# Kernel optimization log

Measured on AMD Instinct MI355X. Metric: run time of the kernel, lower is better.

The kernel has to match this reference:

```python
import jax, jax.numpy as jnp
import numpy as np

EPS = 1e-5

def conv3x3(x, w):
    return jax.lax.conv_general_dilated(x, w, (1, 1), 'SAME', dimension_numbers=('NCHW', 'OIHW', 'NCHW'))

def bn_relu(x, g, b):
    # BatchNorm2d in training mode (batch stats, biased variance), weight=g, bias=b, then ReLU
    m = jnp.mean(x, axis=(0, 2, 3), keepdims=True)
    v = jnp.var(x, axis=(0, 2, 3), keepdims=True)
    return jax.nn.relu((x - m) * jax.lax.rsqrt(v + EPS) * g[None, :, None, None] + b[None, :, None, None])

def conv1x1(x, w, b):
    return jnp.einsum('bchw,oc->bohw', x, w) + b[None, :, None, None]

def cc_core(q, k, v):
    # criss-cross attention core: row (H) + col (W) energies, -inf on H diagonal, joint softmax
    H = q.shape[2]
    eH = jnp.einsum('bchw,bcgw->bhwg', q, k)          # [B,H,W,H]
    eH = jnp.where(jnp.eye(H, dtype=bool)[None, :, None, :], -jnp.inf, eH)
    eW = jnp.einsum('bchw,bchv->bhwv', q, k)          # [B,H,W,W]
    att = jax.nn.softmax(jnp.concatenate([eH, eW], axis=-1), axis=-1)
    aH, aW = att[..., :H], att[..., H:]
    oH = jnp.einsum('bcgw,bhwg->bchw', v, aH)
    oW = jnp.einsum('bchv,bhwv->bchw', v, aW)
    return oH + oW

def cc_attention(x, qw, qb, kw, kb, vw, vb, gamma):
    return gamma * cc_core(conv1x1(x, qw, qb), conv1x1(x, kw, kb), conv1x1(x, vw, vb)) + x

def my_attention(x, qw, qb, kw, kb, vw, vb, gamma):
    # criss-cross attention over the batch rearranged into a (B//4, B//4) grid
    B, C, H, W = x.shape
    g = B // 4  # requires g*g == B (B=16)
    def to_grid(t):
        return t.reshape(B, -1).T.reshape(1, -1, g, g)
    o = cc_core(to_grid(conv1x1(x, qw, qb)), to_grid(conv1x1(x, kw, kb)), to_grid(conv1x1(x, vw, vb)))
    o = o.reshape(-1, B).T.reshape(B, C, H, W)
    return gamma * o + x

RECURRENCE = 2

def setup_inputs() -> dict:
    B, Cin, H, W = 16, 1024, 48, 48
    C = Cin // 4      # 256 (CC_channels == my_channels)
    C8 = C // 8       # 32
    NC, OC = 21, 512
    ks = iter(jax.random.split(jax.random.key(0), 40))
    def rn(shape, s):
        return jax.random.normal(next(ks), shape, jnp.float32) * s
    def attn_params(p):
        return {p + 'q_w': rn((C8, C), 0.06), p + 'q_b': jnp.zeros((C8,)),
                p + 'k_w': rn((C8, C), 0.06), p + 'k_b': jnp.zeros((C8,)),
                p + 'v_w': rn((C, C), 0.06), p + 'v_b': jnp.zeros((C,))}
    inp = {'x': rn((B, Cin, H, W), 1.0),
           'w_a': rn((C, Cin, 3, 3), 0.015), 'g_a': jnp.ones((C,)), 'b_a': jnp.zeros((C,))}
    inp.update(attn_params('cc'))
    inp['cc_gamma'] = jnp.asarray(0.1, jnp.float32)
    inp.update({'w_b': rn((C, C, 3, 3), 0.03), 'g_b': jnp.ones((C,)), 'b_b': jnp.zeros((C,)),
                'w_m1': rn((C, Cin, 3, 3), 0.015), 'g_m1': jnp.ones((C,)), 'b_m1': jnp.zeros((C,))})
    inp.update(attn_params('my'))
    inp['my_gamma'] = jnp.asarray(0.1, jnp.float32)
    inp.update({'w_m2': rn((C, C, 3, 3), 0.03), 'g_m2': jnp.ones((C,)), 'b_m2': jnp.zeros((C,)),
                'w_c': rn((OC, Cin + 2 * C, 3, 3), 0.012), 'g_c': jnp.ones((OC,)), 'b_c': jnp.zeros((OC,)),
                'w_cls': rn((NC, OC), 0.04), 'b_cls': jnp.zeros((NC,))})
    return inp

def reference(x, w_a, g_a, b_a, ccq_w, ccq_b, cck_w, cck_b, ccv_w, ccv_b, cc_gamma,
              w_b, g_b, b_b, w_m1, g_m1, b_m1, myq_w, myq_b, myk_w, myk_b, myv_w, myv_b, my_gamma,
              w_m2, g_m2, b_m2, w_c, g_c, b_c, w_cls, b_cls):
    cc = bn_relu(conv3x3(x, w_a), g_a, b_a)
    my = bn_relu(conv3x3(x, w_m1), g_m1, b_m1)
    for _ in range(RECURRENCE):
        cc = cc_attention(cc, ccq_w, ccq_b, cck_w, cck_b, ccv_w, ccv_b, cc_gamma)
    for _ in range(RECURRENCE):
        my = my_attention(my, myq_w, myq_b, myk_w, myk_b, myv_w, myv_b, my_gamma)
    cc = bn_relu(conv3x3(cc, w_b), g_b, b_b)
    my = bn_relu(conv3x3(my, w_m2), g_m2, b_m2)
    h = bn_relu(conv3x3(jnp.concatenate([x, cc, my], axis=1), w_c), g_c, b_c)
    return conv1x1(h, w_cls, b_cls)
```

## Files before the change

### kernel.cpp

```cpp
#include <hip/hip_runtime.h>
#include <hip/hip_bf16.h>
#include <math.h>

typedef __hip_bfloat16 bf16;
typedef unsigned short ushort;
typedef __attribute__((ext_vector_type(8))) short bh8;
typedef __attribute__((ext_vector_type(4))) float f4;

#define HHW 48
#define PP  2304
#define MM  36864

__device__ __forceinline__ float ldf(const float* p) { return *p; }
__device__ __forceinline__ float ldf(const bf16* p) { return __bfloat162float(*p); }
__device__ __forceinline__ void stf(float* p, float v) { *p = v; }
__device__ __forceinline__ void stf(bf16* p, float v) { *p = __float2bfloat16(v); }
__device__ __forceinline__ float b2f(ushort u) { return __uint_as_float((unsigned)u << 16); }
__device__ __forceinline__ ushort f2bu(float f) { bf16 h = __float2bfloat16(f); return *(ushort*)&h; }

__device__ __forceinline__ int loff(int row, int col8) {
    return row * 32 + (col8 ^ ((((row) >> 1) & 3) << 3));
}

__device__ __forceinline__ void gl_lds(const ushort* g, ushort* l) {
    __builtin_amdgcn_global_load_lds((const __attribute__((address_space(1))) void*)g,
                                     (__attribute__((address_space(3))) void*)l, 16, 0, 0);
}

__global__ void x2b_k(const float* __restrict__ x, bf16* __restrict__ xb) {
    __shared__ float tile[32][33];
    int b  = blockIdx.z;
    int c0 = blockIdx.y * 32;
    int p0 = blockIdx.x * 32;
    int lp = threadIdx.x & 31;
    int cg = threadIdx.x >> 5;
    #pragma unroll
    for (int j = 0; j < 4; ++j) {
        int c = cg * 4 + j;
        tile[c][lp] = x[((size_t)b * 1024 + c0 + c) * PP + p0 + lp];
    }
    __syncthreads();
    #pragma unroll
    for (int j = 0; j < 4; ++j) {
        int rp = cg * 4 + j;
        xb[((size_t)b * PP + p0 + rp) * 1024 + c0 + lp] = __float2bfloat16(tile[lp][rp]);
    }
}

__global__ void w3b_k(const float* __restrict__ w, bf16* __restrict__ wb, int Cout, int Cin) {
    int idx = blockIdx.x * 256 + threadIdx.x;
    int n = Cout * Cin * 9;
    if (idx >= n) return;
    int kk  = idx / (Cout * Cin);
    int rem = idx - kk * Cout * Cin;
    int co  = rem / Cin;
    int ci  = rem - co * Cin;
    wb[idx] = __float2bfloat16(w[((size_t)co * Cin + ci) * 9 + kk]);
}

__global__ void wqkv_k(const float* __restrict__ qw, const float* __restrict__ kw,
                       const float* __restrict__ vw, bf16* __restrict__ dst) {
    int idx = blockIdx.x * 256 + threadIdx.x;
    if (idx >= 320 * 256) return;
    int r = idx >> 8, c = idx & 255;
    float v = (r < 32) ? qw[r * 256 + c] : (r < 64) ? kw[(r - 32) * 256 + c]
                                                    : vw[(size_t)(r - 64) * 256 + c];
    dst[idx] = __float2bfloat16(v);
}

__global__ void cb_k(const float* __restrict__ qb, const float* __restrict__ kb,
                     const float* __restrict__ vb, float* __restrict__ dst) {
    int i = threadIdx.x;
    dst[i] = (i < 32) ? qb[i] : (i < 64) ? kb[i - 32] : vb[i - 64];
}

__global__ void tw1_k(const float* __restrict__ w, float* __restrict__ wt, int O, int Cm) {
    int idx = blockIdx.x * 256 + threadIdx.x;
    int n = O * Cm;
    if (idx >= n) return;
    int o = idx / Cm;
    int c = idx - o * Cm;
    wt[c * O + o] = w[idx];
}

template<typename OutT>
__global__ __launch_bounds__(256, 2)
void mconv3_k(const bf16* __restrict__ in, const bf16* __restrict__ wt,
              const float* __restrict__ bias, OutT* __restrict__ out,
              int Cin, int CinT, int ciOff, int Cout, int accum) {
    __shared__ ushort As[256 * 32];
    __shared__ ushort Bs[384 * 32];
    const ushort* inu = (const ushort*)in;
    const ushort* wtu = (const ushort*)wt;
    int tid = threadIdx.x;
    int N0 = blockIdx.x * 128;
    int M0 = blockIdx.y * 96;
    int sr = tid >> 2;
    int sc = (tid & 3) * 8;
    int wv = tid >> 6, lane = tid & 63;
    int wm = (wv & 1) * 48, wn = (wv >> 1) * 64;
    int l15 = lane & 15, quad = lane >> 4;

    const ushort* aptr[4];
    ushort* alds[4];
    #pragma unroll
    for (int j = 0; j < 4; ++j) {
        int row = j * 64 + sr;
        int scs = sc ^ (((row >> 1) & 3) << 3);
        int gp = M0 - 49 + row;
        gp = gp < 0 ? 0 : (gp > MM - 1 ? MM - 1 : gp);
        aptr[j] = inu + (size_t)gp * Cin + scs;
        alds[j] = As + (j * 64 + wv * 16) * 32;
    }
    const ushort* bptr[6];
    ushort* blds[6];
    #pragma unroll
    for (int j = 0; j < 6; ++j) {
        int row = j * 64 + sr;
        int scs = sc ^ (((row >> 1) & 3) << 3);
        int dxi = row >> 7;
        int crow = row & 127;
        bptr[j] = wtu + ((size_t)dxi * Cout + N0 + crow) * CinT + ciOff + scs;
        blds[j] = Bs + (j * 64 + wv * 16) * 32;
    }
    size_t dystep = (size_t)3 * Cout * CinT;

    int ry[3], rx[3];
    #pragma unroll
    for (int mi = 0; mi < 3; ++mi) {
        int r = (M0 + wm + mi * 16 + l15) % PP;
        ry[mi] = r / HHW;
        rx[mi] = r - ry[mi] * HHW;
    }

    f4 acc[3][4];
    #pragma unroll
    for (int i = 0; i < 3; ++i)
        #pragma unroll
        for (int j = 0; j < 4; ++j) acc[i][j] = (f4){0.f, 0.f, 0.f, 0.f};

    for (int c0 = 0; c0 < Cin; c0 += 32) {
        #pragma unroll
        for (int dy = 0; dy < 3; ++dy) {
            __syncthreads();
            if (dy == 0) {
                #pragma unroll
                for (int j = 0; j < 4; ++j)
                    gl_lds(aptr[j] + c0, alds[j]);
            }
            #pragma unroll
            for (int j = 0; j < 6; ++j)
                gl_lds(bptr[j] + dy * dystep + c0, blds[j]);
            __syncthreads();
            int dyp = dy - 1;
            bool vy[3];
            #pragma unroll
            for (int mi = 0; mi < 3; ++mi) vy[mi] = (unsigned)(ry[mi] + dyp) < (unsigned)HHW;
            #pragma unroll
            for (int dxi = 0; dxi < 3; ++dxi) {
                int dxp = dxi - 1;
                int sh = 49 + dyp * HHW + dxp;
                bh8 af[3], bfr[4];
                #pragma unroll
                for (int mi = 0; mi < 3; ++mi) {
                    bh8 a = {0, 0, 0, 0, 0, 0, 0, 0};
                    if (vy[mi] && (unsigned)(rx[mi] + dxp) < (unsigned)HHW)
                        a = *(const bh8*)(As + loff(wm + mi * 16 + l15 + sh, quad * 8));
                    af[mi] = a;
                }
                #pragma unroll
                for (int ni = 0; ni < 4; ++ni)
                    bfr[ni] = *(const bh8*)(Bs + loff(dxi * 128 + wn + ni * 16 + l15, quad * 8));
                #pragma unroll
                for (int mi = 0; mi < 3; ++mi)
                    #pragma unroll
                    for (int ni = 0; ni < 4; ++ni)
                        acc[mi][ni] = __builtin_amdgcn_mfma_f32_16x16x32_bf16(af[mi], bfr[ni], acc[mi][ni], 0, 0, 0);
            }
        }
    }

    float bvn[4];
    #pragma unroll
    for (int ni = 0; ni < 4; ++ni)
        bvn[ni] = bias ? bias[N0 + wn + ni * 16 + l15] : 0.f;
    #pragma unroll
    for (int mi = 0; mi < 3; ++mi) {
        int mrow = M0 + wm + mi * 16 + quad * 4;
        #pragma unroll
        for (int ni = 0; ni < 4; ++ni) {
            int ncol = N0 + wn + ni * 16 + l15;
            #pragma unroll
            for (int r = 0; r < 4; ++r) {
                size_t oi = (size_t)(mrow + r) * Cout + ncol;
                float val = acc[mi][ni][r] + bvn[ni];
                if (accum) stf(&out[oi], ldf(&out[oi]) + val);
                else       stf(&out[oi], val);
            }
        }
    }
}

__global__ __launch_bounds__(256, 2)
void mqkv_k(const bf16* __restrict__ in, const bf16* __restrict__ wt,
            const float* __restrict__ bias, float* __restrict__ qo,
            float* __restrict__ ko, bf16* __restrict__ vo) {
    __shared__ ushort As[128 * 32];
    __shared__ ushort Bs[64 * 32];
    const int Cin = 256;
    const ushort* inu = (const ushort*)in;
    const ushort* wtu = (const ushort*)wt;
    int tid = threadIdx.x;
    int N0 = blockIdx.x * 64;
    int M0 = blockIdx.y * 96;
    int sr = tid >> 2;
    int sc = (tid & 3) * 8;
    int scs = sc ^ (((sr >> 1) & 3) << 3);
    int wv = tid >> 6, lane = tid & 63;
    int wm = (wv & 1) * 48, wn = (wv >> 1) * 32;
    int l15 = lane & 15, quad = lane >> 4;

    const ushort* aptr[2];
    #pragma unroll
    for (int j = 0; j < 2; ++j) {
        int gp = M0 + j * 64 + sr;
        gp = gp > MM - 1 ? MM - 1 : gp;
        aptr[j] = inu + (size_t)gp * Cin + scs;
    }
    const ushort* bptr = wtu + (size_t)(N0 + sr) * Cin + scs;
    ushort* alds0 = As + (wv * 16) * 32;
    ushort* alds1 = As + (64 + wv * 16) * 32;
    ushort* blds  = Bs + (wv * 16) * 32;

    f4 acc[3][2];
    #pragma unroll
    for (int i = 0; i < 3; ++i)
        #pragma unroll
        for (int j = 0; j < 2; ++j) acc[i][j] = (f4){0.f, 0.f, 0.f, 0.f};

    for (int c0 = 0; c0 < Cin; c0 += 32) {
        __syncthreads();
        gl_lds(aptr[0] + c0, alds0);
        gl_lds(aptr[1] + c0, alds1);
        gl_lds(bptr + c0, blds);
        __syncthreads();
        bh8 af[3], bfr[2];
        #pragma unroll
        for (int mi = 0; mi < 3; ++mi)
            af[mi] = *(const bh8*)(As + loff(wm + mi * 16 + l15, quad * 8));
        #pragma unroll
        for (int ni = 0; ni < 2; ++ni)
            bfr[ni] = *(const bh8*)(Bs + loff(wn + ni * 16 + l15, quad * 8));
        #pragma unroll
        for (int mi = 0; mi < 3; ++mi)
            #pragma unroll
            for (int ni = 0; ni < 2; ++ni)
                acc[mi][ni] = __builtin_amdgcn_mfma_f32_16x16x32_bf16(af[mi], bfr[ni], acc[mi][ni], 0, 0, 0);
    }

    float bvn[2];
    #pragma unroll
    for (int ni = 0; ni < 2; ++ni)
        bvn[ni] = bias[N0 + wn + ni * 16 + l15];
    #pragma unroll
    for (int mi = 0; mi < 3; ++mi) {
        int mrow = M0 + wm + mi * 16 + quad * 4;
        #pragma unroll
        for (int ni = 0; ni < 2; ++ni) {
            int ncol = N0 + wn + ni * 16 + l15;
            #pragma unroll
            for (int r = 0; r < 4; ++r) {
                float val = acc[mi][ni][r] + bvn[ni];
                if (ncol < 32)
                    qo[(size_t)(mrow + r) * 32 + ncol] = val;
                else if (ncol < 64)
                    ko[(size_t)(mrow + r) * 32 + ncol - 32] = val;
                else
                    vo[(size_t)(mrow + r) * 256 + ncol - 64] = __float2bfloat16(val);
            }
        }
    }
}

__global__ void zero_k(float* p, int n) {
    int i = blockIdx.x * 256 + threadIdx.x;
    if (i < n) p[i] = 0.f;
}

template<typename S>
__global__ void bn_stats_k(const S* __restrict__ src, float* __restrict__ sum,
                           float* __restrict__ sumsq, int Cout) {
    int t  = threadIdx.x;
    int c  = blockIdx.x * 64 + (t & 63);
    int pl = t >> 6;
    int p0 = blockIdx.y * 1024;
    float s = 0.f, ss = 0.f;
    for (int i = pl; i < 1024; i += 4) {
        float v = ldf(&src[(size_t)(p0 + i) * Cout + c]);
        s += v; ss += v * v;
    }
    __shared__ float ls[256], lss[256];
    ls[t] = s; lss[t] = ss;
    __syncthreads();
    if (t < 64) {
        s  = ls[t]  + ls[t + 64]  + ls[t + 128]  + ls[t + 192];
        ss = lss[t] + lss[t + 64] + lss[t + 128] + lss[t + 192];
        atomicAdd(&sum[c], s);
        atomicAdd(&sumsq[c], ss);
    }
}

__global__ void bn_fin_k(const float* __restrict__ sum, const float* __restrict__ sumsq,
                         const float* __restrict__ g, const float* __restrict__ b,
                         float* __restrict__ scale, float* __restrict__ shift, int Cout) {
    int c = blockIdx.x * 256 + threadIdx.x;
    if (c >= Cout) return;
    const float invM = 1.f / 36864.f;
    float mean = sum[c] * invM;
    float var  = sumsq[c] * invM - mean * mean;
    float inv  = 1.f / sqrtf(var + 1e-5f);
    scale[c] = g[c] * inv;
    shift[c] = b[c] - mean * g[c] * inv;
}

template<typename S, typename D>
__global__ void bn_apply_k(const S* __restrict__ src, const float* __restrict__ scale,
                           const float* __restrict__ shift, D* __restrict__ dst,
                           int cmask, int n) {
    int idx = blockIdx.x * 256 + threadIdx.x;
    if (idx >= n) return;
    int c = idx & cmask;
    float y = ldf(&src[idx]) * scale[c] + shift[c];
    stf(&dst[idx], fmaxf(y, 0.f));
}

__global__ void cc_logits_k(const float* __restrict__ q, const float* __restrict__ kk,
                            float* __restrict__ att) {
    int t = threadIdx.x;
    int p = blockIdx.x;
    int b = p / PP;
    int r = p - b * PP;
    int h = r / HHW;
    int w = r - h * HHW;
    __shared__ float qv[32];
    if (t < 32) qv[t] = q[p * 32 + t];
    __syncthreads();
    float val = -INFINITY;
    if (t < 48) {
        if (t != h) {
            const float* kr = kk + ((b * HHW + t) * HHW + w) * 32;
            float s = 0.f;
            #pragma unroll
            for (int c = 0; c < 32; ++c) s += qv[c] * kr[c];
            val = s;
        }
    } else if (t < 96) {
        const float* kr = kk + ((b * HHW + h) * HHW + (t - 48)) * 32;
        float s = 0.f;
        #pragma unroll
        for (int c = 0; c < 32; ++c) s += qv[c] * kr[c];
        val = s;
    }
    __shared__ float red[128];
    red[t] = val;
    __syncthreads();
    for (int st = 64; st > 0; st >>= 1) { if (t < st) red[t] = fmaxf(red[t], red[t + st]); __syncthreads(); }
    float m = red[0];
    __syncthreads();
    float e = (t < 96 && val != -INFINITY) ? expf(val - m) : 0.f;
    red[t] = e;
    __syncthreads();
    for (int st = 64; st > 0; st >>= 1) { if (t < st) red[t] += red[t + st]; __syncthreads(); }
    float inv = 1.f / red[0];
    if (t < 96) att[p * 96 + t] = e * inv;
}

__global__ void cc_out_k(const float* __restrict__ att, const bf16* __restrict__ v,
                         bf16* __restrict__ cc, const float* __restrict__ gptr) {
    int t = threadIdx.x;
    int p = blockIdx.x;
    __shared__ float a[96];
    if (t < 96) a[t] = att[p * 96 + t];
    __syncthreads();
    int b = p / PP;
    int r = p - b * PP;
    int h = r / HHW;
    int w = r - h * HHW;
    const ushort* vb = (const ushort*)v + (size_t)b * PP * 256;
    int c2 = t * 2;
    float a0 = 0.f, a1 = 0.f;
    #pragma unroll 4
    for (int g = 0; g < 48; ++g) {
        unsigned u = *(const unsigned*)&vb[(g * HHW + w) * 256 + c2];
        a0 += a[g] * b2f((ushort)u);
        a1 += a[g] * b2f((ushort)(u >> 16));
    }
    #pragma unroll 4
    for (int tt = 0; tt < 48; ++tt) {
        unsigned u = *(const unsigned*)&vb[(h * HHW + tt) * 256 + c2];
        a0 += a[48 + tt] * b2f((ushort)u);
        a1 += a[48 + tt] * b2f((ushort)(u >> 16));
    }
    float gamma = gptr[0];
    unsigned* cp = (unsigned*)((ushort*)cc + (size_t)p * 256 + c2);
    unsigned old = *cp;
    float r0 = gamma * a0 + b2f((ushort)old);
    float r1 = gamma * a1 + b2f((ushort)(old >> 16));
    *cp = (unsigned)f2bu(r0) | ((unsigned)f2bu(r1) << 16);
}

__global__ void gram_k(const float* __restrict__ q, const float* __restrict__ k,
                       float* __restrict__ G) {
    int t = threadIdx.x;
    int a  = blockIdx.x >> 4;
    int b2 = blockIdx.x & 15;
    const float* qa = q + a * 73728;
    const float* kb = k + b2 * 73728;
    float s = 0.f;
    for (int i = t; i < 73728; i += 256) s += qa[i] * kb[i];
    __shared__ float red[256];
    red[t] = s;
    __syncthreads();
    for (int st = 128; st > 0; st >>= 1) { if (t < st) red[t] += red[t + st]; __syncthreads(); }
    if (t == 0) G[blockIdx.x] = red[0];
}

__global__ void my_soft_k(const float* __restrict__ G, float* __restrict__ A) {
    int t = threadIdx.x;
    if (t >= 16) return;
    int i = t >> 2, j = t & 3;
    float l[8];
    for (int g = 0; g < 4; ++g) l[g] = (g == i) ? -INFINITY : G[t * 16 + g * 4 + j];
    for (int v = 0; v < 4; ++v) l[4 + v] = G[t * 16 + i * 4 + v];
    float m = l[0];
    for (int n = 1; n < 8; ++n) m = fmaxf(m, l[n]);
    float s = 0.f;
    for (int n = 0; n < 8; ++n) { l[n] = expf(l[n] - m); s += l[n]; }
    float inv = 1.f / s;
    for (int n = 0; n < 8; ++n) A[t * 8 + n] = l[n] * inv;
}

__global__ void my_out_k(const float* __restrict__ A, const bf16* __restrict__ v,
                         bf16* __restrict__ my, const float* __restrict__ gptr) {
    int t = threadIdx.x;
    __shared__ float As[128];
    if (t < 128) As[t] = A[t];
    __syncthreads();
    size_t pidx = (size_t)blockIdx.x * 256 + t;
    size_t idx = pidx * 2;
    int b = (int)(idx / 589824);
    int n = (int)(idx - (size_t)b * 589824);
    int i = b >> 2, j = b & 3;
    const ushort* vu = (const ushort*)v;
    float o0 = 0.f, o1 = 0.f;
    #pragma unroll
    for (int g = 0; g < 4; ++g) {
        unsigned u = *(const unsigned*)&vu[(size_t)(g * 4 + j) * 589824 + n];
        o0 += As[b * 8 + g] * b2f((ushort)u);
        o1 += As[b * 8 + g] * b2f((ushort)(u >> 16));
    }
    #pragma unroll
    for (int tt = 0; tt < 4; ++tt) {
        unsigned u = *(const unsigned*)&vu[(size_t)(i * 4 + tt) * 589824 + n];
        o0 += As[b * 8 + 4 + tt] * b2f((ushort)u);
        o1 += As[b * 8 + 4 + tt] * b2f((ushort)(u >> 16));
    }
    float gamma = gptr[0];
    unsigned* mp = (unsigned*)((ushort*)my + idx);
    unsigned old = *mp;
    float r0 = gamma * o0 + b2f((ushort)old);
    float r1 = gamma * o1 + b2f((ushort)(old >> 16));
    *mp = (unsigned)f2bu(r0) | ((unsigned)f2bu(r1) << 16);
}

__global__ void cls_k(const float* __restrict__ hsrc, const float* __restrict__ wt,
                      const float* __restrict__ bias, float* __restrict__ out) {
    int t = threadIdx.x;
    int p = blockIdx.x;
    __shared__ float hr[512];
    for (int i = t; i < 512; i += 128) hr[i] = hsrc[(size_t)p * 512 + i];
    __syncthreads();
    if (t < 21) {
        float acc = bias[t];
        #pragma unroll 4
        for (int c = 0; c < 512; ++c) acc += hr[c] * wt[c * 21 + t];
        int b = p / PP;
        int r = p - b * PP;
        out[(b * 21 + t) * PP + r] = acc;
    }
}

extern "C" void kernel_launch(void* const* d_in, const int* in_sizes, int n_in,
                              void* d_out, int out_size, void* d_ws, size_t ws_size,
                              hipStream_t stream) {
    const float* x     = (const float*)d_in[0];
    const float* w_a   = (const float*)d_in[1];
    const float* g_a   = (const float*)d_in[2];
    const float* b_a   = (const float*)d_in[3];
    const float* ccq_w = (const float*)d_in[4];
    const float* ccq_b = (const float*)d_in[5];
    const float* cck_w = (const float*)d_in[6];
    const float* cck_b = (const float*)d_in[7];
    const float* ccv_w = (const float*)d_in[8];
    const float* ccv_b = (const float*)d_in[9];
    const float* cc_g  = (const float*)d_in[10];
    const float* w_b   = (const float*)d_in[11];
    const float* g_b   = (const float*)d_in[12];
    const float* b_b   = (const float*)d_in[13];
    const float* w_m1  = (const float*)d_in[14];
    const float* g_m1  = (const float*)d_in[15];
    const float* b_m1  = (const float*)d_in[16];
    const float* myq_w = (const float*)d_in[17];
    const float* myq_b = (const float*)d_in[18];
    const float* myk_w = (const float*)d_in[19];
    const float* myk_b = (const float*)d_in[20];
    const float* myv_w = (const float*)d_in[21];
    const float* myv_b = (const float*)d_in[22];
    const float* my_g  = (const float*)d_in[23];
    const float* w_m2  = (const float*)d_in[24];
    const float* g_m2  = (const float*)d_in[25];
    const float* b_m2  = (const float*)d_in[26];
    const float* w_c   = (const float*)d_in[27];
    const float* g_c   = (const float*)d_in[28];
    const float* b_c   = (const float*)d_in[29];
    const float* w_cls = (const float*)d_in[30];
    const float* b_cls = (const float*)d_in[31];
    float* out = (float*)d_out;

    char* ws = (char*)d_ws;
    size_t off = 0;
    bf16* cc  = (bf16*)(ws + off); off += (size_t)MM * 256 * 2;
    bf16* my  = (bf16*)(ws + off); off += (size_t)MM * 256 * 2;
    char* hx  = ws + off;          off += (size_t)MM * 256 * 4;
    char* B   = ws + off;          off += (size_t)MM * 512 * 4;
    bf16* wab  = (bf16*)(ws + off); off += 4718592;
    bf16* wm1b = (bf16*)(ws + off); off += 4718592;
    bf16* wbb  = (bf16*)(ws + off); off += 1179648;
    bf16* wm2b = (bf16*)(ws + off); off += 1179648;
    bf16* wcb  = (bf16*)(ws + off); off += 14155776;
    bf16* wqc  = (bf16*)(ws + off); off += 163840;
    bf16* wqm  = (bf16*)(ws + off); off += 163840;
    float* wclsT = (float*)(ws + off); off += 43008;
    float* stats = (float*)(ws + off); off += 16384;
    if (ws_size < off) return;
    float* ssum   = stats;
    float* ssumsq = stats + 512;
    float* sscale = stats + 1024;
    float* sshift = stats + 1536;
    float* G = stats + 2048;
    float* A = stats + 2048 + 256;
    float* bqc = stats + 2560;
    float* bqm = stats + 2880;

    bf16*  xbf = (bf16*)B;
    float* qb  = (float*)B;
    float* kb  = (float*)(B + 4718592);
    bf16*  vbb = (bf16*)(B + 9437184);
    float* att = (float*)(B + 47185920);
    float* hxf = (float*)hx;
    bf16*  hxb = (bf16*)hx;
    float* hfin = (float*)B;

    x2b_k<<<dim3(72, 32, 16), 256, 0, stream>>>(x, xbf);
    w3b_k<<<9216, 256, 0, stream>>>(w_a,  wab,  256, 1024);
    w3b_k<<<9216, 256, 0, stream>>>(w_m1, wm1b, 256, 1024);
    w3b_k<<<2304, 256, 0, stream>>>(w_b,  wbb,  256, 256);
    w3b_k<<<2304, 256, 0, stream>>>(w_m2, wm2b, 256, 256);
    w3b_k<<<27648, 256, 0, stream>>>(w_c, wcb,  512, 1536);
    wqkv_k<<<320, 256, 0, stream>>>(ccq_w, cck_w, ccv_w, wqc);
    wqkv_k<<<320, 256, 0, stream>>>(myq_w, myk_w, myv_w, wqm);
    cb_k<<<1, 320, 0, stream>>>(ccq_b, cck_b, ccv_b, bqc);
    cb_k<<<1, 320, 0, stream>>>(myq_b, myk_b, myv_b, bqm);
    tw1_k<<<42, 256, 0, stream>>>(w_cls, wclsT, 21, 512);

    auto bn = [&](auto* src, const float* g, const float* b, auto* dst, int Cout) {
        zero_k<<<4, 256, 0, stream>>>(ssum, 1024);
        bn_stats_k<<<dim3(Cout / 64, 36), 256, 0, stream>>>(src, ssum, ssumsq, Cout);
        bn_fin_k<<<(Cout + 255) / 256, 256, 0, stream>>>(ssum, ssumsq, g, b, sscale, sshift, Cout);
        int n = MM * Cout;
        bn_apply_k<<<n / 256, 256, 0, stream>>>(src, sscale, sshift, dst, Cout - 1, n);
    };

    mconv3_k<float><<<dim3(2, 384), 256, 0, stream>>>(xbf, wab, nullptr, hxf, 1024, 1024, 0, 256, 0);
    bn(hxf, g_a, b_a, cc, 256);
    mconv3_k<float><<<dim3(2, 384), 256, 0, stream>>>(xbf, wm1b, nullptr, hxf, 1024, 1024, 0, 256, 0);
    bn(hxf, g_m1, b_m1, my, 256);
    mconv3_k<bf16><<<dim3(4, 384), 256, 0, stream>>>(xbf, wcb, nullptr, hxb, 1024, 1536, 0, 512, 0);

    for (int rec = 0; rec < 2; ++rec) {
        mqkv_k<<<dim3(5, 384), 256, 0, stream>>>(cc, wqc, bqc, qb, kb, vbb);
        cc_logits_k<<<MM, 128, 0, stream>>>(qb, kb, att);
        cc_out_k<<<MM, 128, 0, stream>>>(att, vbb, cc, cc_g);
    }

    for (int rec = 0; rec < 2; ++rec) {
        mqkv_k<<<dim3(5, 384), 256, 0, stream>>>(my, wqm, bqm, qb, kb, vbb);
        gram_k<<<256, 256, 0, stream>>>(qb, kb, G);
        my_soft_k<<<1, 64, 0, stream>>>(G, A);
        my_out_k<<<18432, 256, 0, stream>>>(A, vbb, my, my_g);
    }

    float* pscr = (float*)B;
    mconv3_k<float><<<dim3(2, 384), 256, 0, stream>>>(cc, wbb, nullptr, pscr, 256, 256, 0, 256, 0);
    bn(pscr, g_b, b_b, cc, 256);
    mconv3_k<float><<<dim3(2, 384), 256, 0, stream>>>(my, wm2b, nullptr, pscr, 256, 256, 0, 256, 0);
    bn(pscr, g_m2, b_m2, my, 256);

    mconv3_k<bf16><<<dim3(4, 384), 256, 0, stream>>>(cc, wcb, nullptr, hxb, 256, 1536, 1024, 512, 1);
    mconv3_k<bf16><<<dim3(4, 384), 256, 0, stream>>>(my, wcb, nullptr, hxb, 256, 1536, 1280, 512, 1);
    bn(hxb, g_c, b_c, hfin, 512);

    cls_k<<<MM, 128, 0, stream>>>(hfin, wclsT, b_cls, out);
}
```

Measured before the change: 2.792 ms.

## Split criss-cross output into LDS-tiled H/W passes and retile conv/qkv kernels

The per-pixel criss-cross output kernel is replaced by two kernels that stage a whole column or row of V and the matching attention weights in LDS. Each block then reuses that data across 48 pixels instead of re-reading V from global memory for every pixel, at the cost of a bf16 intermediate buffer written and read between the passes. The qkv GEMM tile grows from 96 to 128 rows, which makes the M clamp unnecessary. The 3x3 conv skips the unused fourth A-tile load for the last wave and replaces the branchy zero fill with a read from a zeroed LDS row. The logits kernel loads K with float4 vector loads.

```diff
diff --git a/kernel.cpp b/kernel.cpp
--- a/kernel.cpp
+++ b/kernel.cpp
@@ -101,6 +101,11 @@
     int wm = (wv & 1) * 48, wn = (wv >> 1) * 64;
     int l15 = lane & 15, quad = lane >> 4;
 
+    if (tid < 4) {
+        uint4 z; z.x = z.y = z.z = z.w = 0;
+        *(uint4*)(As + 255 * 32 + tid * 8) = z;
+    }
+
     const ushort* aptr[4];
     ushort* alds[4];
     #pragma unroll
@@ -146,7 +151,8 @@
             if (dy == 0) {
                 #pragma unroll
                 for (int j = 0; j < 4; ++j)
-                    gl_lds(aptr[j] + c0, alds[j]);
+                    if (j < 3 || wv < 3)
+                        gl_lds(aptr[j] + c0, alds[j]);
             }
             #pragma unroll
             for (int j = 0; j < 6; ++j)
@@ -163,10 +169,10 @@
                 bh8 af[3], bfr[4];
                 #pragma unroll
                 for (int mi = 0; mi < 3; ++mi) {
-                    bh8 a = {0, 0, 0, 0, 0, 0, 0, 0};
-                    if (vy[mi] && (unsigned)(rx[mi] + dxp) < (unsigned)HHW)
-                        a = *(const bh8*)(As + loff(wm + mi * 16 + l15 + sh, quad * 8));
-                    af[mi] = a;
+                    bool vld = vy[mi] && ((unsigned)(rx[mi] + dxp) < (unsigned)HHW);
+                    int ad = vld ? loff(wm + mi * 16 + l15 + sh, quad * 8)
+                                 : (255 * 32 + quad * 8);
+                    af[mi] = *(const bh8*)(As + ad);
                 }
                 #pragma unroll
                 for (int ni = 0; ni < 4; ++ni)
@@ -212,29 +218,26 @@
     const ushort* wtu = (const ushort*)wt;
     int tid = threadIdx.x;
     int N0 = blockIdx.x * 64;
-    int M0 = blockIdx.y * 96;
+    int M0 = blockIdx.y * 128;
     int sr = tid >> 2;
     int sc = (tid & 3) * 8;
     int scs = sc ^ (((sr >> 1) & 3) << 3);
     int wv = tid >> 6, lane = tid & 63;
-    int wm = (wv & 1) * 48, wn = (wv >> 1) * 32;
+    int wm = (wv & 1) * 64, wn = (wv >> 1) * 32;
     int l15 = lane & 15, quad = lane >> 4;
 
     const ushort* aptr[2];
     #pragma unroll
-    for (int j = 0; j < 2; ++j) {
-        int gp = M0 + j * 64 + sr;
-        gp = gp > MM - 1 ? MM - 1 : gp;
-        aptr[j] = inu + (size_t)gp * Cin + scs;
-    }
+    for (int j = 0; j < 2; ++j)
+        aptr[j] = inu + (size_t)(M0 + j * 64 + sr) * Cin + scs;
     const ushort* bptr = wtu + (size_t)(N0 + sr) * Cin + scs;
     ushort* alds0 = As + (wv * 16) * 32;
     ushort* alds1 = As + (64 + wv * 16) * 32;
     ushort* blds  = Bs + (wv * 16) * 32;
 
-    f4 acc[3][2];
-    #pragma unroll
-    for (int i = 0; i < 3; ++i)
+    f4 acc[4][2];
+    #pragma unroll
+    for (int i = 0; i < 4; ++i)
         #pragma unroll
         for (int j = 0; j < 2; ++j) acc[i][j] = (f4){0.f, 0.f, 0.f, 0.f};
 
@@ -244,15 +247,15 @@
         gl_lds(aptr[1] + c0, alds1);
         gl_lds(bptr + c0, blds);
         __syncthreads();
-        bh8 af[3], bfr[2];
-        #pragma unroll
-        for (int mi = 0; mi < 3; ++mi)
+        bh8 af[4], bfr[2];
+        #pragma unroll
+        for (int mi = 0; mi < 4; ++mi)
             af[mi] = *(const bh8*)(As + loff(wm + mi * 16 + l15, quad * 8));
         #pragma unroll
         for (int ni = 0; ni < 2; ++ni)
             bfr[ni] = *(const bh8*)(Bs + loff(wn + ni * 16 + l15, quad * 8));
         #pragma unroll
-        for (int mi = 0; mi < 3; ++mi)
+        for (int mi = 0; mi < 4; ++mi)
             #pragma unroll
             for (int ni = 0; ni < 2; ++ni)
                 acc[mi][ni] = __builtin_amdgcn_mfma_f32_16x16x32_bf16(af[mi], bfr[ni], acc[mi][ni], 0, 0, 0);
@@ -263,7 +266,7 @@
     for (int ni = 0; ni < 2; ++ni)
         bvn[ni] = bias[N0 + wn + ni * 16 + l15];
     #pragma unroll
-    for (int mi = 0; mi < 3; ++mi) {
+    for (int mi = 0; mi < 4; ++mi) {
         int mrow = M0 + wm + mi * 16 + quad * 4;
         #pragma unroll
         for (int ni = 0; ni < 2; ++ni) {
@@ -348,17 +351,25 @@
     float val = -INFINITY;
     if (t < 48) {
         if (t != h) {
-            const float* kr = kk + ((b * HHW + t) * HHW + w) * 32;
+            const float4* kr4 = (const float4*)(kk + ((b * HHW + t) * HHW + w) * 32);
             float s = 0.f;
             #pragma unroll
-            for (int c = 0; c < 32; ++c) s += qv[c] * kr[c];
+            for (int c = 0; c < 8; ++c) {
+                float4 kv = kr4[c];
+                s += qv[c * 4 + 0] * kv.x + qv[c * 4 + 1] * kv.y
+                   + qv[c * 4 + 2] * kv.z + qv[c * 4 + 3] * kv.w;
+            }
             val = s;
         }
     } else if (t < 96) {
-        const float* kr = kk + ((b * HHW + h) * HHW + (t - 48)) * 32;
+        const float4* kr4 = (const float4*)(kk + ((b * HHW + h) * HHW + (t - 48)) * 32);
         float s = 0.f;
         #pragma unroll
-        for (int c = 0; c < 32; ++c) s += qv[c] * kr[c];
+        for (int c = 0; c < 8; ++c) {
+            float4 kv = kr4[c];
+            s += qv[c * 4 + 0] * kv.x + qv[c * 4 + 1] * kv.y
+               + qv[c * 4 + 2] * kv.z + qv[c * 4 + 3] * kv.w;
+        }
         val = s;
     }
     __shared__ float red[128];
@@ -375,38 +386,77 @@
     if (t < 96) att[p * 96 + t] = e * inv;
 }
 
-__global__ void cc_out_k(const float* __restrict__ att, const bf16* __restrict__ v,
-                         bf16* __restrict__ cc, const float* __restrict__ gptr) {
+__global__ void ccH_k(const float* __restrict__ att, const bf16* __restrict__ v,
+                      bf16* __restrict__ tmp) {
+    __shared__ ushort vs[48][256];
+    __shared__ float as_[48][48];
+    int w = blockIdx.x, b = blockIdx.y;
     int t = threadIdx.x;
-    int p = blockIdx.x;
-    __shared__ float a[96];
-    if (t < 96) a[t] = att[p * 96 + t];
-    __syncthreads();
-    int b = p / PP;
-    int r = p - b * PP;
-    int h = r / HHW;
-    int w = r - h * HHW;
-    const ushort* vb = (const ushort*)v + (size_t)b * PP * 256;
-    int c2 = t * 2;
-    float a0 = 0.f, a1 = 0.f;
-    #pragma unroll 4
-    for (int g = 0; g < 48; ++g) {
-        unsigned u = *(const unsigned*)&vb[(g * HHW + w) * 256 + c2];
-        a0 += a[g] * b2f((ushort)u);
-        a1 += a[g] * b2f((ushort)(u >> 16));
-    }
-    #pragma unroll 4
-    for (int tt = 0; tt < 48; ++tt) {
-        unsigned u = *(const unsigned*)&vb[(h * HHW + tt) * 256 + c2];
-        a0 += a[48 + tt] * b2f((ushort)u);
-        a1 += a[48 + tt] * b2f((ushort)(u >> 16));
-    }
+    const ushort* vu = (const ushort*)v + ((size_t)b * PP + w) * 256;
+    for (int i = t; i < 48 * 32; i += 256) {
+        int g = i >> 5, c8 = (i & 31) * 8;
+        *(bh8*)&vs[g][c8] = *(const bh8*)(vu + (size_t)g * HHW * 256 + c8);
+    }
+    for (int i = t; i < 48 * 48; i += 256) {
+        int h = i / 48, g = i - h * 48;
+        as_[h][g] = att[((size_t)(b * PP + h * HHW + w)) * 96 + g];
+    }
+    __syncthreads();
+    int c2 = (t & 127) * 2;
+    int h0 = (t >> 7) * 24;
+    for (int hh = 0; hh < 24; ++hh) {
+        int h = h0 + hh;
+        float o0 = 0.f, o1 = 0.f;
+        #pragma unroll 4
+        for (int g = 0; g < 48; ++g) {
+            float a = as_[h][g];
+            unsigned u = *(const unsigned*)&vs[g][c2];
+            o0 += a * b2f((ushort)u);
+            o1 += a * b2f((ushort)(u >> 16));
+        }
+        unsigned* tp = (unsigned*)((ushort*)tmp + ((size_t)(b * PP + h * HHW + w)) * 256 + c2);
+        *tp = (unsigned)f2bu(o0) | ((unsigned)f2bu(o1) << 16);
+    }
+}
+
+__global__ void ccW_k(const float* __restrict__ att, const bf16* __restrict__ v,
+                      const bf16* __restrict__ tmp, bf16* __restrict__ cc,
+                      const float* __restrict__ gptr) {
+    __shared__ ushort vs[48][256];
+    __shared__ float as_[48][48];
+    int h = blockIdx.x, b = blockIdx.y;
+    int t = threadIdx.x;
+    const ushort* vu = (const ushort*)v + ((size_t)b * PP + h * HHW) * 256;
+    for (int i = t; i < 48 * 32; i += 256) {
+        int tt = i >> 5, c8 = (i & 31) * 8;
+        *(bh8*)&vs[tt][c8] = *(const bh8*)(vu + (size_t)tt * 256 + c8);
+    }
+    for (int i = t; i < 48 * 48; i += 256) {
+        int w = i / 48, tt = i - w * 48;
+        as_[w][tt] = att[((size_t)(b * PP + h * HHW + w)) * 96 + 48 + tt];
+    }
+    __syncthreads();
     float gamma = gptr[0];
-    unsigned* cp = (unsigned*)((ushort*)cc + (size_t)p * 256 + c2);
-    unsigned old = *cp;
-    float r0 = gamma * a0 + b2f((ushort)old);
-    float r1 = gamma * a1 + b2f((ushort)(old >> 16));
-    *cp = (unsigned)f2bu(r0) | ((unsigned)f2bu(r1) << 16);
+    int c2 = (t & 127) * 2;
+    int w0 = (t >> 7) * 24;
+    for (int ww = 0; ww < 24; ++ww) {
+        int w = w0 + ww;
+        float o0 = 0.f, o1 = 0.f;
+        #pragma unroll 4
+        for (int tt = 0; tt < 48; ++tt) {
+            float a = as_[w][tt];
+            unsigned u = *(const unsigned*)&vs[tt][c2];
+            o0 += a * b2f((ushort)u);
+            o1 += a * b2f((ushort)(u >> 16));
+        }
+        size_t base = ((size_t)(b * PP + h * HHW + w)) * 256 + c2;
+        unsigned ut = *(const unsigned*)((const ushort*)tmp + base);
+        unsigned* cp = (unsigned*)((ushort*)cc + base);
+        unsigned old = *cp;
+        float r0 = gamma * (o0 + b2f((ushort)ut)) + b2f((ushort)old);
+        float r1 = gamma * (o1 + b2f((ushort)(ut >> 16))) + b2f((ushort)(old >> 16));
+        *cp = (unsigned)f2bu(r0) | ((unsigned)f2bu(r1) << 16);
+    }
 }
 
 __global__ void gram_k(const float* __restrict__ q, const float* __restrict__ k,
@@ -556,6 +606,7 @@
     float* qb  = (float*)B;
     float* kb  = (float*)(B + 4718592);
     bf16*  vbb = (bf16*)(B + 9437184);
+    bf16*  tmpH = (bf16*)(B + 28311552);
     float* att = (float*)(B + 47185920);
     float* hxf = (float*)hx;
     bf16*  hxb = (bf16*)hx;
@@ -588,13 +639,14 @@
     mconv3_k<bf16><<<dim3(4, 384), 256, 0, stream>>>(xbf, wcb, nullptr, hxb, 1024, 1536, 0, 512, 0);
 
     for (int rec = 0; rec < 2; ++rec) {
-        mqkv_k<<<dim3(5, 384), 256, 0, stream>>>(cc, wqc, bqc, qb, kb, vbb);
+        mqkv_k<<<dim3(5, 288), 256, 0, stream>>>(cc, wqc, bqc, qb, kb, vbb);
         cc_logits_k<<<MM, 128, 0, stream>>>(qb, kb, att);
-        cc_out_k<<<MM, 128, 0, stream>>>(att, vbb, cc, cc_g);
+        ccH_k<<<dim3(48, 16), 256, 0, stream>>>(att, vbb, tmpH);
+        ccW_k<<<dim3(48, 16), 256, 0, stream>>>(att, vbb, tmpH, cc, cc_g);
     }
 
     for (int rec = 0; rec < 2; ++rec) {
-        mqkv_k<<<dim3(5, 384), 256, 0, stream>>>(my, wqm, bqm, qb, kb, vbb);
+        mqkv_k<<<dim3(5, 288), 256, 0, stream>>>(my, wqm, bqm, qb, kb, vbb);
         gram_k<<<256, 256, 0, stream>>>(qb, kb, G);
         my_soft_k<<<1, 64, 0, stream>>>(G, A);
         my_out_k<<<18432, 256, 0, stream>>>(A, vbb, my, my_g);
```

Measured after the change: 2.524 ms. -9.6%, faster.
